# Kernel optimization log

Measured on AMD Instinct MI355X. Metric: run time of the kernel, lower is better.

Reference implementation:

```python
import jax, jax.numpy as jnp
import numpy as np

HIDDEN = 32          # config.model_hidden_channels
KSIZE = 3            # dilated conv kernel size
DIL = 3              # dilated conv dilation
SLOPE = 0.2          # leaky relu slope

B, L = 16, 32768
HOP = 256
KL = L // HOP        # kernel_length = 128
LVC_K = 3            # location-variable conv kernel size
OUT = 2 * HIDDEN     # gated output channels


def _leaky(x):
    return jnp.where(x >= 0, x, SLOPE * x)


def setup_inputs() -> dict:
    key = jax.random.key(0)
    k1, k2, k3, k4, k5 = jax.random.split(key, 5)
    return {
        "hidden_states": jax.random.normal(k1, (B, HIDDEN, L), dtype=jnp.float32),
        "kernel": jax.random.normal(k2, (B, HIDDEN, OUT, LVC_K, KL), dtype=jnp.float32) * 0.1,
        "bias": jax.random.normal(k3, (B, OUT, KL), dtype=jnp.float32) * 0.1,
        "conv_w": jax.random.normal(k4, (HIDDEN, HIDDEN, KSIZE), dtype=jnp.float32) * (1.0 / np.sqrt(HIDDEN * KSIZE)),
        "conv_b": jax.random.normal(k5, (HIDDEN,), dtype=jnp.float32) * 0.01,
        "hop_size": HOP,
    }


def reference(hidden_states, kernel, bias, conv_w, conv_b, hop_size):
    residual = hidden_states
    x = _leaky(hidden_states)
    # dilated Conv1d, 'same' padding
    pad = DIL * (KSIZE - 1) // 2
    x = jax.lax.conv_general_dilated(
        x, conv_w, window_strides=(1,), padding=[(pad, pad)],
        rhs_dilation=(DIL,), dimension_numbers=("NCH", "OIH", "NCH"))
    x = x + conv_b[None, :, None]
    x = _leaky(x)

    # location-variable convolution (dilation=1 path of the torch code)
    b, c, in_len = x.shape
    _, _, out_ch, k, kl = kernel.shape
    p = (k - 1) // 2
    xp = jnp.pad(x, ((0, 0), (0, 0), (p, p)))           # (B, C, L+2p)
    # sliding windows of size k at every position (equivalent of the unfolds)
    idx = jnp.arange(in_len)[:, None] + jnp.arange(k)[None, :]   # (L, k)
    win = xp[:, :, idx]                                  # (B, C, L, k)
    win = win.reshape(b, c, kl, hop_size, k)             # (B, C, KL, hop, k)
    # per-segment local GEMM: einsum 'bildsk,biokl->bolsd' with d==1
    out = jnp.einsum("bilsk,biokl->bols", win, kernel)   # (B, O, KL, hop)
    out = out + bias[:, :, :, None]
    out = out.reshape(b, out_ch, in_len)                 # (B, 2C, L)

    # gated activation + residual
    y = jax.nn.sigmoid(out[:, :HIDDEN, :]) * jnp.tanh(out[:, HIDDEN:, :])
    return residual + y
```

## Files before the change

### kernel.cpp

```cpp
#include <hip/hip_runtime.h>

static constexpr int HID = 32;
static constexpr int LEN = 32768;
static constexpr int NKL = 128;
static constexpr int HOP = 256;
#define SLOPE 0.2f

typedef short short8 __attribute__((ext_vector_type(8)));
typedef float floatx4 __attribute__((ext_vector_type(4)));

static constexpr int XROW  = 80;
static constexpr int WOFF  = 22400;
static constexpr int OSROW = 528;
static constexpr int SMEMB = 34688;

__device__ __forceinline__ float leaky(float x) { return x >= 0.0f ? x : SLOPE * x; }

__device__ __forceinline__ unsigned short f2bf(float f) {
    union { float f; unsigned u; } v; v.f = f;
    unsigned r = v.u + 0x7FFFu + ((v.u >> 16) & 1u);
    return (unsigned short)(r >> 16);
}
__device__ __forceinline__ float bf2f(unsigned short s) {
    union { unsigned u; float f; } v; v.u = ((unsigned)s) << 16;
    return v.f;
}
__device__ __forceinline__ float gatef(float a, float c) {
    c = fminf(fmaxf(c, -20.0f), 20.0f);
    float sg = 1.0f / (1.0f + __expf(-a));
    float e2 = __expf(-2.0f * c);
    return sg * (1.0f - e2) / (1.0f + e2);
}

__global__ __launch_bounds__(256, 3) void univnet_mfma(
    const float* __restrict__ h,
    const float* __restrict__ kern,
    const float* __restrict__ bias,
    const float* __restrict__ cw,
    const float* __restrict__ cb,
    float* __restrict__ out)
{
    __shared__ __align__(16) char smem[SMEMB];

    const int blk = blockIdx.x;
    const int b   = blk & 15;
    const int kl  = blk >> 4;
    const int t0  = kl * HOP;
    const int p0  = t0 - 4;
    const int tid = threadIdx.x;
    const int w   = tid >> 6;
    const int lane = tid & 63;
    const int l15 = lane & 15;
    const int l4  = lane >> 4;

    const float* hb = h + (size_t)b * (HID * LEN);
    const bool edge = (kl == 0) || (kl == NKL - 1);

    {
        auto stage = [&](int tau) {
            const int oct = tau & 3, cq = tau >> 2;
            union { unsigned short u[8]; short8 v; } sh[4];
            if (!edge) {
                #pragma unroll
                for (int j = 0; j < 8; ++j) {
                    const int i = oct * 8 + j;
                    float4 f = *(const float4*)(hb + (size_t)i * LEN + p0 + 4 * cq);
                    sh[0].u[j] = f2bf(leaky(f.x));
                    sh[1].u[j] = f2bf(leaky(f.y));
                    sh[2].u[j] = f2bf(leaky(f.z));
                    sh[3].u[j] = f2bf(leaky(f.w));
                }
            } else {
                #pragma unroll
                for (int j = 0; j < 8; ++j) {
                    const int i = oct * 8 + j;
                    #pragma unroll
                    for (int e = 0; e < 4; ++e) {
                        int p = p0 + 4 * cq + e;
                        float v = 0.0f;
                        if (p >= 0 && p < LEN) v = leaky(hb[(size_t)i * LEN + p]);
                        sh[e].u[j] = f2bf(v);
                    }
                }
            }
            #pragma unroll
            for (int e = 0; e < 4; ++e)
                *(short8*)(smem + (4 * cq + e) * XROW + oct * 16) = sh[e].v;
        };
        stage(tid);
        if (tid < 8) stage(256 + tid);
        for (int z = tid; z < 320; z += 256)
            ((unsigned*)(smem + 264 * XROW))[z] = 0u;
    }

    #pragma unroll
    for (int j = 0; j < 12; ++j) {
        int e = tid + 256 * j;
        float v = cw[e];
        int o = e / 96; int rem = e - o * 96;
        int i = rem / 3; int kk = rem - i * 3;
        *(unsigned short*)(smem + WOFF + (o * 96 + kk * 32 + i) * 2) = f2bf(v);
    }

    const int ib2 = tid >> 3, oo8 = tid & 7;
    float kreg[24];
    {
        const float* kbase = kern + (((size_t)b * 32 + ib2) * 64) * 3 * 128 + kl;
        #pragma unroll
        for (int u = 0; u < 8; ++u)
            #pragma unroll
            for (int kk = 0; kk < 3; ++kk)
                kreg[u * 3 + kk] = kbase[(size_t)((oo8 * 8 + u) * 3 + kk) * 128];
    }

    __syncthreads();

    short8 b1f[2][3];
    #pragma unroll
    for (int tn = 0; tn < 2; ++tn)
        #pragma unroll
        for (int qk = 0; qk < 3; ++qk)
            b1f[tn][qk] = *(const short8*)(smem + WOFF +
                              ((tn * 16 + l15) * 96 + qk * 32 + l4 * 8) * 2);
    const float cbv0 = cb[l15], cbv1 = cb[16 + l15];

    floatx4 cacc[9];
    #pragma unroll
    for (int n = 0; n < 9; ++n) {
        const int tt = w + 4 * n;
        if (tt < 34) {
            const int tm = tt >> 1, tn = tt & 1;
            short8 af[3];
            #pragma unroll
            for (int qk = 0; qk < 3; ++qk)
                af[qk] = *(const short8*)(smem + (tm * 16 + l15 + 3 * qk) * XROW + l4 * 16);
            const float bv = tn ? cbv1 : cbv0;
            floatx4 acc = {bv, bv, bv, bv};
            #pragma unroll
            for (int qk = 0; qk < 3; ++qk)
                acc = __builtin_amdgcn_mfma_f32_16x16x32_bf16(af[qk], b1f[tn][qk], acc, 0, 0, 0);
            cacc[n] = acc;
        }
    }
    __syncthreads();

    #pragma unroll
    for (int n = 0; n < 9; ++n) {
        const int tt = w + 4 * n;
        if (tt < 34) {
            const int tm = tt >> 1, tn = tt & 1;
            const int ich = tn * 16 + l15;
            #pragma unroll
            for (int r = 0; r < 4; ++r) {
                const int c_out = tm * 16 + l4 * 4 + r;
                const int p = t0 - 1 + c_out;
                unsigned short v = ((unsigned)p < (unsigned)LEN) ? f2bf(leaky(cacc[n][r])) : 0;
                *(unsigned short*)(smem + c_out * XROW + ich * 2) = v;
            }
        }
    }
    #pragma unroll
    for (int u = 0; u < 8; ++u)
        #pragma unroll
        for (int kk = 0; kk < 3; ++kk) {
            const int o = oo8 * 8 + u;
            *(unsigned short*)(smem + WOFF + (o * 96 + kk * 32 + ib2) * 2) =
                f2bf(kreg[u * 3 + kk]);
        }
    __syncthreads();

    unsigned garr[2][4][2];
    #pragma unroll
    for (int pp = 0; pp < 2; ++pp) {
        const int oA = pp * 16 + l15, oB = oA + 32;
        short8 b2A[3], b2B[3];
        #pragma unroll
        for (int qk = 0; qk < 3; ++qk) {
            b2A[qk] = *(const short8*)(smem + WOFF + (oA * 96 + qk * 32 + l4 * 8) * 2);
            b2B[qk] = *(const short8*)(smem + WOFF + (oB * 96 + qk * 32 + l4 * 8) * 2);
        }
        const float bA = bias[((size_t)b * 64 + oA) * NKL + kl];
        const float bB = bias[((size_t)b * 64 + oB) * NKL + kl];
        #pragma unroll
        for (int t = 0; t < 4; ++t) {
            const int tm = 4 * t + w;
            short8 af[3];
            #pragma unroll
            for (int qk = 0; qk < 3; ++qk)
                af[qk] = *(const short8*)(smem + (tm * 16 + l15 + qk) * XROW + l4 * 16);
            floatx4 aA = {bA, bA, bA, bA}, aB = {bB, bB, bB, bB};
            #pragma unroll
            for (int qk = 0; qk < 3; ++qk) {
                aA = __builtin_amdgcn_mfma_f32_16x16x32_bf16(af[qk], b2A[qk], aA, 0, 0, 0);
                aB = __builtin_amdgcn_mfma_f32_16x16x32_bf16(af[qk], b2B[qk], aB, 0, 0, 0);
            }
            #pragma unroll
            for (int hp = 0; hp < 2; ++hp) {
                unsigned g0 = f2bf(gatef(aA[2 * hp],     aB[2 * hp]));
                unsigned g1 = f2bf(gatef(aA[2 * hp + 1], aB[2 * hp + 1]));
                garr[pp][t][hp] = g0 | (g1 << 16);
            }
        }
    }
    __syncthreads();

    #pragma unroll
    for (int pp = 0; pp < 2; ++pp) {
        const int o = pp * 16 + l15;
        #pragma unroll
        for (int t = 0; t < 4; ++t) {
            const int sbase = (4 * t + w) * 16 + l4 * 4;
            #pragma unroll
            for (int hp = 0; hp < 2; ++hp)
                *(unsigned*)(smem + o * OSROW + (sbase + 2 * hp) * 2) = garr[pp][t][hp];
        }
    }
    __syncthreads();

    {
        const int eo = tid >> 3, e8 = tid & 7;
        const float* hrow = hb + (size_t)eo * LEN + t0;
        float* orow = out + ((size_t)b * HID + eo) * LEN + t0;
        #pragma unroll
        for (int rep = 0; rep < 8; ++rep) {
            const int s = e8 * 4 + 32 * rep;
            uint2 g = *(const uint2*)(smem + eo * OSROW + s * 2);
            float4 hv = *(const float4*)(hrow + s);
            float4 ov;
            ov.x = hv.x + bf2f((unsigned short)(g.x & 0xffff));
            ov.y = hv.y + bf2f((unsigned short)(g.x >> 16));
            ov.z = hv.z + bf2f((unsigned short)(g.y & 0xffff));
            ov.w = hv.w + bf2f((unsigned short)(g.y >> 16));
            *(float4*)(orow + s) = ov;
        }
    }
}

extern "C" void kernel_launch(void* const* d_in, const int* in_sizes, int n_in,
                              void* d_out, int out_size, void* d_ws, size_t ws_size,
                              hipStream_t stream) {
    const float* h    = (const float*)d_in[0];
    const float* kern = (const float*)d_in[1];
    const float* bias = (const float*)d_in[2];
    const float* cw   = (const float*)d_in[3];
    const float* cb   = (const float*)d_in[4];
    float* outp = (float*)d_out;

    univnet_mfma<<<2048, 256, 0, stream>>>(h, kern, bias, cw, cb, outp);
}
```

Baseline: 248.1 us.

## Pre-transpose LVC kernel to bf16 slabs in a prep kernel and DMA into LDS

Adds a prep kernel that converts the location-variable kernel and conv weights to bf16 and lays them out as one contiguous padded slab per (batch, segment) in the workspace. The main kernel then loads each slab straight into LDS with global_load_lds, replacing the strided scalar gathers and per-element transposed LDS writes it did before. It also swaps the MFMA operand order for the first conv so each lane holds packed outputs, and uses v_cvt_pk_bf16_f32 for paired conversions. The cost is an extra launch and a full read-write pass over the kernel tensor through the workspace.

```diff
diff --git a/kernel.cpp b/kernel.cpp
--- a/kernel.cpp
+++ b/kernel.cpp
@@ -8,13 +8,19 @@
 
 typedef short short8 __attribute__((ext_vector_type(8)));
 typedef float floatx4 __attribute__((ext_vector_type(4)));
+typedef unsigned int u32;
 
 static constexpr int XROW  = 80;
 static constexpr int WOFF  = 22400;
+static constexpr int WROW  = 208;
+static constexpr int WSLAB = 64 * WROW;
 static constexpr int OSROW = 528;
-static constexpr int SMEMB = 34688;
-
-__device__ __forceinline__ float leaky(float x) { return x >= 0.0f ? x : SLOPE * x; }
+static constexpr int SMEMB = WOFF + WSLAB;
+
+static constexpr size_t KT_USH  = (size_t)16 * NKL * 64 * 104;
+static constexpr size_t CWT_OFF = KT_USH;
+
+__device__ __forceinline__ float leaky(float x) { return fmaxf(x, SLOPE * x); }
 
 __device__ __forceinline__ unsigned short f2bf(float f) {
     union { float f; unsigned u; } v; v.f = f;
@@ -24,6 +30,11 @@
 __device__ __forceinline__ float bf2f(unsigned short s) {
     union { unsigned u; float f; } v; v.u = ((unsigned)s) << 16;
     return v.f;
+}
+__device__ __forceinline__ u32 cvtpk(float lo, float hi) {
+    u32 r;
+    asm("v_cvt_pk_bf16_f32 %0, %1, %2" : "=v"(r) : "v"(lo), "v"(hi));
+    return r;
 }
 __device__ __forceinline__ float gatef(float a, float c) {
     c = fminf(fmaxf(c, -20.0f), 20.0f);
@@ -32,13 +43,59 @@
     return sg * (1.0f - e2) / (1.0f + e2);
 }
 
+__global__ __launch_bounds__(256) void prep_kern(
+    const float* __restrict__ kern,
+    const float* __restrict__ cw,
+    unsigned short* __restrict__ kt)
+{
+    const int blk = blockIdx.x;
+    const int b = blk >> 6, o = blk & 63;
+    const int tid = threadIdx.x;
+    __shared__ unsigned short lt[32 * 384];
+
+    const float* src = kern + (size_t)(b * 2048 + o) * 384;
+    #pragma unroll
+    for (int j = 0; j < 12; ++j) {
+        const int f = tid + 256 * j;
+        const int i = f / 96, r = f - i * 96;
+        float4 v = *(const float4*)(src + (size_t)i * 24576 + (size_t)r * 4);
+        uint2 pk2 = make_uint2(cvtpk(v.x, v.y), cvtpk(v.z, v.w));
+        *(uint2*)(lt + i * 384 + r * 4) = pk2;
+    }
+
+    if (blk == 0) {
+        #pragma unroll
+        for (int j = 0; j < 12; ++j) {
+            const int d = tid + 256 * j;
+            const int o2 = d / 96, rr = d - o2 * 96;
+            const int kk = rr >> 5, i = rr & 31;
+            kt[CWT_OFF + d] = f2bf(cw[(o2 * 32 + i) * 3 + kk]);
+        }
+    }
+    __syncthreads();
+
+    const int kl = tid >> 1, half = tid & 1;
+    u32 wbuf[24];
+    #pragma unroll
+    for (int m = 0; m < 24; ++m) {
+        const int c0 = half * 48 + 2 * m;
+        const int kk = c0 >> 5, i0 = c0 & 31;
+        u32 lo = lt[i0 * 384 + kk * 128 + kl];
+        u32 hi = lt[(i0 + 1) * 384 + kk * 128 + kl];
+        wbuf[m] = lo | (hi << 16);
+    }
+    unsigned short* dst = kt + ((size_t)(b * NKL + kl) * 64 + o) * 104 + half * 48;
+    #pragma unroll
+    for (int m = 0; m < 6; ++m)
+        ((uint4*)dst)[m] = make_uint4(wbuf[4*m], wbuf[4*m+1], wbuf[4*m+2], wbuf[4*m+3]);
+}
+
 __global__ __launch_bounds__(256, 3) void univnet_mfma(
     const float* __restrict__ h,
-    const float* __restrict__ kern,
     const float* __restrict__ bias,
-    const float* __restrict__ cw,
     const float* __restrict__ cb,
-    float* __restrict__ out)
+    float* __restrict__ out,
+    const unsigned short* __restrict__ kt)
 {
     __shared__ __align__(16) char smem[SMEMB];
 
@@ -57,72 +114,78 @@
     const bool edge = (kl == 0) || (kl == NKL - 1);
 
     {
+        const char* slab = (const char*)kt + (size_t)(b * NKL + kl) * WSLAB;
+        #pragma unroll
+        for (int j = 0; j < 4; ++j) {
+            const int c = w + 4 * j;
+            if (c < 13)
+                __builtin_amdgcn_global_load_lds(
+                    (const u32 __attribute__((address_space(1)))*)(slab + c * 1024 + lane * 16),
+                    (u32 __attribute__((address_space(3)))*)(smem + WOFF + c * 1024),
+                    16, 0, 0);
+        }
+    }
+
+    const unsigned short* cwt = kt + CWT_OFF;
+    short8 b1f[2][3];
+    #pragma unroll
+    for (int tn = 0; tn < 2; ++tn)
+        #pragma unroll
+        for (int qk = 0; qk < 3; ++qk)
+            b1f[tn][qk] = *(const short8*)(cwt + (tn * 16 + l15) * 96 + qk * 32 + l4 * 8);
+    float4 cbq[2];
+    cbq[0] = *(const float4*)(cb + l4 * 4);
+    cbq[1] = *(const float4*)(cb + 16 + l4 * 4);
+    float bv[2][2];
+    #pragma unroll
+    for (int pp = 0; pp < 2; ++pp) {
+        bv[pp][0] = bias[((size_t)b * 64 + pp * 16 + l15) * NKL + kl];
+        bv[pp][1] = bias[((size_t)b * 64 + pp * 16 + l15 + 32) * NKL + kl];
+    }
+
+    {
         auto stage = [&](int tau) {
             const int oct = tau & 3, cq = tau >> 2;
-            union { unsigned short u[8]; short8 v; } sh[4];
+            u32 pk[4][4];
             if (!edge) {
                 #pragma unroll
-                for (int j = 0; j < 8; ++j) {
-                    const int i = oct * 8 + j;
-                    float4 f = *(const float4*)(hb + (size_t)i * LEN + p0 + 4 * cq);
-                    sh[0].u[j] = f2bf(leaky(f.x));
-                    sh[1].u[j] = f2bf(leaky(f.y));
-                    sh[2].u[j] = f2bf(leaky(f.z));
-                    sh[3].u[j] = f2bf(leaky(f.w));
+                for (int jp = 0; jp < 4; ++jp) {
+                    const int i0 = oct * 8 + 2 * jp;
+                    float4 f0 = *(const float4*)(hb + (size_t)i0 * LEN + p0 + 4 * cq);
+                    float4 f1 = *(const float4*)(hb + (size_t)(i0 + 1) * LEN + p0 + 4 * cq);
+                    pk[0][jp] = cvtpk(leaky(f0.x), leaky(f1.x));
+                    pk[1][jp] = cvtpk(leaky(f0.y), leaky(f1.y));
+                    pk[2][jp] = cvtpk(leaky(f0.z), leaky(f1.z));
+                    pk[3][jp] = cvtpk(leaky(f0.w), leaky(f1.w));
                 }
             } else {
                 #pragma unroll
-                for (int j = 0; j < 8; ++j) {
-                    const int i = oct * 8 + j;
+                for (int jp = 0; jp < 4; ++jp) {
+                    const int i0 = oct * 8 + 2 * jp;
                     #pragma unroll
                     for (int e = 0; e < 4; ++e) {
-                        int p = p0 + 4 * cq + e;
-                        float v = 0.0f;
-                        if (p >= 0 && p < LEN) v = leaky(hb[(size_t)i * LEN + p]);
-                        sh[e].u[j] = f2bf(v);
+                        const int p = p0 + 4 * cq + e;
+                        float a = 0.0f, c2 = 0.0f;
+                        if ((unsigned)p < (unsigned)LEN) {
+                            a  = leaky(hb[(size_t)i0 * LEN + p]);
+                            c2 = leaky(hb[(size_t)(i0 + 1) * LEN + p]);
+                        }
+                        pk[e][jp] = cvtpk(a, c2);
                     }
                 }
             }
             #pragma unroll
             for (int e = 0; e < 4; ++e)
-                *(short8*)(smem + (4 * cq + e) * XROW + oct * 16) = sh[e].v;
+                *(uint4*)(smem + (4 * cq + e) * XROW + oct * 16) =
+                    make_uint4(pk[e][0], pk[e][1], pk[e][2], pk[e][3]);
         };
         stage(tid);
         if (tid < 8) stage(256 + tid);
         for (int z = tid; z < 320; z += 256)
-            ((unsigned*)(smem + 264 * XROW))[z] = 0u;
-    }
-
-    #pragma unroll
-    for (int j = 0; j < 12; ++j) {
-        int e = tid + 256 * j;
-        float v = cw[e];
-        int o = e / 96; int rem = e - o * 96;
-        int i = rem / 3; int kk = rem - i * 3;
-        *(unsigned short*)(smem + WOFF + (o * 96 + kk * 32 + i) * 2) = f2bf(v);
-    }
-
-    const int ib2 = tid >> 3, oo8 = tid & 7;
-    float kreg[24];
-    {
-        const float* kbase = kern + (((size_t)b * 32 + ib2) * 64) * 3 * 128 + kl;
-        #pragma unroll
-        for (int u = 0; u < 8; ++u)
-            #pragma unroll
-            for (int kk = 0; kk < 3; ++kk)
-                kreg[u * 3 + kk] = kbase[(size_t)((oo8 * 8 + u) * 3 + kk) * 128];
-    }
-
-    __syncthreads();
-
-    short8 b1f[2][3];
-    #pragma unroll
-    for (int tn = 0; tn < 2; ++tn)
-        #pragma unroll
-        for (int qk = 0; qk < 3; ++qk)
-            b1f[tn][qk] = *(const short8*)(smem + WOFF +
-                              ((tn * 16 + l15) * 96 + qk * 32 + l4 * 8) * 2);
-    const float cbv0 = cb[l15], cbv1 = cb[16 + l15];
+            ((u32*)(smem + 264 * XROW))[z] = 0u;
+    }
+
+    __syncthreads();
 
     floatx4 cacc[9];
     #pragma unroll
@@ -134,11 +197,10 @@
             #pragma unroll
             for (int qk = 0; qk < 3; ++qk)
                 af[qk] = *(const short8*)(smem + (tm * 16 + l15 + 3 * qk) * XROW + l4 * 16);
-            const float bv = tn ? cbv1 : cbv0;
-            floatx4 acc = {bv, bv, bv, bv};
+            floatx4 acc = {cbq[tn].x, cbq[tn].y, cbq[tn].z, cbq[tn].w};
             #pragma unroll
             for (int qk = 0; qk < 3; ++qk)
-                acc = __builtin_amdgcn_mfma_f32_16x16x32_bf16(af[qk], b1f[tn][qk], acc, 0, 0, 0);
+                acc = __builtin_amdgcn_mfma_f32_16x16x32_bf16(b1f[tn][qk], af[qk], acc, 0, 0, 0);
             cacc[n] = acc;
         }
     }
@@ -149,24 +211,16 @@
         const int tt = w + 4 * n;
         if (tt < 34) {
             const int tm = tt >> 1, tn = tt & 1;
-            const int ich = tn * 16 + l15;
-            #pragma unroll
-            for (int r = 0; r < 4; ++r) {
-                const int c_out = tm * 16 + l4 * 4 + r;
-                const int p = t0 - 1 + c_out;
-                unsigned short v = ((unsigned)p < (unsigned)LEN) ? f2bf(leaky(cacc[n][r])) : 0;
-                *(unsigned short*)(smem + c_out * XROW + ich * 2) = v;
+            const int c_out = tm * 16 + l15;
+            const int p = t0 - 1 + c_out;
+            u32 q0 = 0u, q1 = 0u;
+            if ((unsigned)p < (unsigned)LEN) {
+                q0 = cvtpk(leaky(cacc[n][0]), leaky(cacc[n][1]));
+                q1 = cvtpk(leaky(cacc[n][2]), leaky(cacc[n][3]));
             }
-        }
-    }
-    #pragma unroll
-    for (int u = 0; u < 8; ++u)
-        #pragma unroll
-        for (int kk = 0; kk < 3; ++kk) {
-            const int o = oo8 * 8 + u;
-            *(unsigned short*)(smem + WOFF + (o * 96 + kk * 32 + ib2) * 2) =
-                f2bf(kreg[u * 3 + kk]);
-        }
+            *(uint2*)(smem + c_out * XROW + (tn * 16 + l4 * 4) * 2) = make_uint2(q0, q1);
+        }
+    }
     __syncthreads();
 
     unsigned garr[2][4][2];
@@ -176,11 +230,10 @@
         short8 b2A[3], b2B[3];
         #pragma unroll
         for (int qk = 0; qk < 3; ++qk) {
-            b2A[qk] = *(const short8*)(smem + WOFF + (oA * 96 + qk * 32 + l4 * 8) * 2);
-            b2B[qk] = *(const short8*)(smem + WOFF + (oB * 96 + qk * 32 + l4 * 8) * 2);
-        }
-        const float bA = bias[((size_t)b * 64 + oA) * NKL + kl];
-        const float bB = bias[((size_t)b * 64 + oB) * NKL + kl];
+            b2A[qk] = *(const short8*)(smem + WOFF + oA * WROW + (qk * 32 + l4 * 8) * 2);
+            b2B[qk] = *(const short8*)(smem + WOFF + oB * WROW + (qk * 32 + l4 * 8) * 2);
+        }
+        const float bA = bv[pp][0], bB = bv[pp][1];
         #pragma unroll
         for (int t = 0; t < 4; ++t) {
             const int tm = 4 * t + w;
@@ -195,11 +248,9 @@
                 aB = __builtin_amdgcn_mfma_f32_16x16x32_bf16(af[qk], b2B[qk], aB, 0, 0, 0);
             }
             #pragma unroll
-            for (int hp = 0; hp < 2; ++hp) {
-                unsigned g0 = f2bf(gatef(aA[2 * hp],     aB[2 * hp]));
-                unsigned g1 = f2bf(gatef(aA[2 * hp + 1], aB[2 * hp + 1]));
-                garr[pp][t][hp] = g0 | (g1 << 16);
-            }
+            for (int hp = 0; hp < 2; ++hp)
+                garr[pp][t][hp] =
+                    cvtpk(gatef(aA[2 * hp], aB[2 * hp]), gatef(aA[2 * hp + 1], aB[2 * hp + 1]));
         }
     }
     __syncthreads();
@@ -212,7 +263,7 @@
             const int sbase = (4 * t + w) * 16 + l4 * 4;
             #pragma unroll
             for (int hp = 0; hp < 2; ++hp)
-                *(unsigned*)(smem + o * OSROW + (sbase + 2 * hp) * 2) = garr[pp][t][hp];
+                *(u32*)(smem + o * OSROW + (sbase + 2 * hp) * 2) = garr[pp][t][hp];
         }
     }
     __syncthreads();
@@ -245,6 +296,8 @@
     const float* cw   = (const float*)d_in[3];
     const float* cb   = (const float*)d_in[4];
     float* outp = (float*)d_out;
-
-    univnet_mfma<<<2048, 256, 0, stream>>>(h, kern, bias, cw, cb, outp);
-}
+    unsigned short* kt = (unsigned short*)d_ws;
+
+    prep_kern<<<1024, 256, 0, stream>>>(kern, cw, kt);
+    univnet_mfma<<<2048, 256, 0, stream>>>(h, bias, cb, outp, kt);
+}
```

After: 229.0 us. 7.7% less time.
